# Kernel optimization log

Hardware: AMD Instinct MI355X
Metric: run time of the kernel (lower is better)

## Reference

```python
import jax, jax.numpy as jnp
import numpy as np

BLOCK = 16          # NVFP4 block size along contraction dim
FP4_MAX = 6.0       # max magnitude of E2M1
FP8_MAX = 448.0     # max magnitude of float8_e4m3fn

_LEVELS = jnp.array([0.0, 0.5, 1.0, 1.5, 2.0, 3.0, 4.0, 6.0], dtype=jnp.float32)
_MIDS   = jnp.array([0.25, 0.75, 1.25, 1.75, 2.5, 3.5, 5.0], dtype=jnp.float32)


def quantize_dequant_nvfp4(t, global_scale):
    """Fake-quantize t (last dim % 16 == 0) to NVFP4: per-16-block fp8-e4m3
    scale times global fp32 scale, values snapped to the E2M1 grid."""
    shp = t.shape
    tb = t.reshape(shp[:-1] + (shp[-1] // BLOCK, BLOCK))
    amax = jnp.max(jnp.abs(tb), axis=-1, keepdims=True)
    # per-block scale, quantized to float8_e4m3fn as in TensorCoreNVFP4Layout
    bs = amax / (FP4_MAX * global_scale)
    bs8 = bs.astype(jnp.float8_e4m3fn).astype(jnp.float32)
    scale = bs8 * global_scale                       # effective dequant scale
    v = tb / jnp.maximum(scale, 1e-12)
    sign = jnp.sign(v)
    a = jnp.clip(jnp.abs(v), 0.0, FP4_MAX)
    idx = jnp.sum(a[..., None] > _MIDS, axis=-1)     # nearest E2M1 level
    q = _LEVELS[idx] * sign * scale
    return q.reshape(shp)


def setup_inputs() -> dict:
    key = jax.random.key(0)
    kx, kw, kb = jax.random.split(key, 3)
    x = jax.random.normal(kx, (8192, 4096), dtype=jnp.float32)
    weight = jax.random.normal(kw, (4096, 4096), dtype=jnp.float32) * 0.02
    bias = jax.random.normal(kb, (4096,), dtype=jnp.float32) * 0.02
    # global scales (weight_scale_2 / input_scale): amax / (6 * 448)
    input_scale = jnp.max(jnp.abs(x)) / (FP4_MAX * FP8_MAX)
    weight_scale = jnp.max(jnp.abs(weight)) / (FP4_MAX * FP8_MAX)
    return {"x": x, "weight": weight, "bias": bias,
            "input_scale": input_scale, "weight_scale": weight_scale}


def reference(x, weight, bias, input_scale, weight_scale):
    xq = quantize_dequant_nvfp4(x, input_scale)      # [T, K]
    wq = quantize_dequant_nvfp4(weight, weight_scale)  # [N, K]
    return jnp.einsum('tk,nk->tn', xq, wq) + bias    # F.linear
```

## Files before the change

### kernel.cpp

```cpp
#include <hip/hip_runtime.h>
#include <hip/hip_bf16.h>
#include <stdint.h>

typedef __attribute__((ext_vector_type(8))) __bf16 bf16x8;
typedef __attribute__((ext_vector_type(4))) float f32x4;

#define BM 256
#define BN 256
#define BKT 32
#define RING 4
#define SLOT_BYTES 16384


__device__ __forceinline__ float fp8_e4m3_rne(float x) {
  if (x < 0.015625f) {
    return rintf(x * 512.0f) * 0.001953125f;
  }
  uint32_t u = __float_as_uint(x);
  uint32_t keep = u & 0xFFF00000u;
  uint32_t rem  = u & 0x000FFFFFu;
  uint32_t lsb  = (u >> 20) & 1u;
  if (rem > 0x80000u || (rem == 0x80000u && lsb)) keep += 0x100000u;
  return __uint_as_float(keep);
}

__device__ __forceinline__ float snap_lvl(float a) {
  if (a > 5.0f)  return 6.0f;
  if (a > 3.5f)  return 4.0f;
  if (a > 2.5f)  return 3.0f;
  if (a > 1.75f) return 2.0f;
  if (a > 1.25f) return 1.5f;
  if (a > 0.75f) return 1.0f;
  if (a > 0.25f) return 0.5f;
  return 0.0f;
}

__global__ __launch_bounds__(256) void quant_nvfp4(
    const float* __restrict__ in, unsigned short* __restrict__ out,
    const float* __restrict__ gsp, int nblk) {
  int b = blockIdx.x * 256 + threadIdx.x;
  if (b >= nblk) return;
  float gs = gsp[0];
  const float4* p = reinterpret_cast<const float4*>(in) + (size_t)b * 4;
  float v[16];
#pragma unroll
  for (int i = 0; i < 4; ++i) {
    float4 t4 = p[i];
    v[i * 4 + 0] = t4.x; v[i * 4 + 1] = t4.y;
    v[i * 4 + 2] = t4.z; v[i * 4 + 3] = t4.w;
  }
  float amax = 0.0f;
#pragma unroll
  for (int i = 0; i < 16; ++i) amax = fmaxf(amax, fabsf(v[i]));
  float bs8 = fp8_e4m3_rne(amax / (6.0f * gs));
  float scale = fmaxf(bs8 * gs, 1e-12f);
  unsigned short o[16];
#pragma unroll
  for (int i = 0; i < 16; ++i) {
    float q = v[i] / scale;
    float a = fminf(fabsf(q), 6.0f);
    float val = copysignf(snap_lvl(a) * bs8, q);
    o[i] = (unsigned short)(__float_as_uint(val) >> 16);
  }
  uint4 w0 = make_uint4((uint32_t)o[0] | ((uint32_t)o[1] << 16),
                        (uint32_t)o[2] | ((uint32_t)o[3] << 16),
                        (uint32_t)o[4] | ((uint32_t)o[5] << 16),
                        (uint32_t)o[6] | ((uint32_t)o[7] << 16));
  uint4 w1 = make_uint4((uint32_t)o[8]  | ((uint32_t)o[9]  << 16),
                        (uint32_t)o[10] | ((uint32_t)o[11] << 16),
                        (uint32_t)o[12] | ((uint32_t)o[13] << 16),
                        (uint32_t)o[14] | ((uint32_t)o[15] << 16));
  uint4* op = reinterpret_cast<uint4*>(out + (size_t)b * 16);
  op[0] = w0;
  op[1] = w1;
}


__device__ __forceinline__ void async_lds16(const void* g, void* l) {
  __builtin_amdgcn_global_load_lds((__attribute__((address_space(1))) void*)(g),
                                   (__attribute__((address_space(3))) void*)(l),
                                   16, 0, 0);
}

#define PHASE0(T, DO_STAGE) {                                                  \
    const char* _ab = (const char*)As + ((T) & 3) * SLOT_BYTES;                \
    const char* _bb = (const char*)Bs + ((T) & 3) * SLOT_BYTES;                \
    _Pragma("unroll") for (int mi = 0; mi < 4; ++mi)                           \
      af[mi] = *(const bf16x8*)(_ab + offA[mi]);                               \
    _Pragma("unroll") for (int ni = 0; ni < 4; ++ni)                           \
      bfr[ni] = *(const bf16x8*)(_bb + offB[ni]);                              \
    if (DO_STAGE) {                                                            \
      char* _la = (char*)As + (((T) + 3) & 3) * SLOT_BYTES;                    \
      char* _lb = (char*)Bs + (((T) + 3) & 3) * SLOT_BYTES;                    \
      async_lds16(pA0 + (size_t)((T) + 3) * BKT, _la + lo0);                   \
      async_lds16(pB0 + (size_t)((T) + 3) * BKT, _lb + lo0);                   \
    }                                                                          \
    __builtin_amdgcn_s_barrier();                                              \
    asm volatile("s_waitcnt lgkmcnt(0)" ::: "memory");                         \
    __builtin_amdgcn_sched_barrier(0);                                         \
    __builtin_amdgcn_s_setprio(1);                                             \
    _Pragma("unroll") for (int mi = 0; mi < 4; ++mi)                           \
      _Pragma("unroll") for (int ni = 0; ni < 4; ++ni)                         \
        acc[mi][ni] = __builtin_amdgcn_mfma_f32_16x16x32_bf16(                 \
            af[mi], bfr[ni], acc[mi][ni], 0, 0, 0);                            \
    __builtin_amdgcn_s_setprio(0);                                             \
    __builtin_amdgcn_sched_barrier(0);                                         \
    __builtin_amdgcn_s_barrier();                                              \
  }

#define PHASE1(T, DO_STAGE, VMASM) {                                           \
    const char* _ab = (const char*)As + ((T) & 3) * SLOT_BYTES;                \
    _Pragma("unroll") for (int mi = 0; mi < 4; ++mi)                           \
      af[mi] = *(const bf16x8*)(_ab + offA[4 + mi]);                           \
    if (DO_STAGE) {                                                            \
      char* _la = (char*)As + (((T) + 3) & 3) * SLOT_BYTES;                    \
      char* _lb = (char*)Bs + (((T) + 3) & 3) * SLOT_BYTES;                    \
      async_lds16(pA1 + (size_t)((T) + 3) * BKT, _la + lo1);                   \
      async_lds16(pB1 + (size_t)((T) + 3) * BKT, _lb + lo1);                   \
    }                                                                          \
    VMASM;                                                                     \
    __builtin_amdgcn_s_barrier();                                              \
    asm volatile("s_waitcnt lgkmcnt(0)" ::: "memory");                         \
    __builtin_amdgcn_sched_barrier(0);                                         \
    __builtin_amdgcn_s_setprio(1);                                             \
    _Pragma("unroll") for (int mi = 0; mi < 4; ++mi)                           \
      _Pragma("unroll") for (int ni = 0; ni < 4; ++ni)                         \
        acc[4 + mi][ni] = __builtin_amdgcn_mfma_f32_16x16x32_bf16(             \
            af[mi], bfr[ni], acc[4 + mi][ni], 0, 0, 0);                        \
    __builtin_amdgcn_s_setprio(0);                                             \
    __builtin_amdgcn_sched_barrier(0);                                         \
    __builtin_amdgcn_s_barrier();                                              \
  }

#define STAGE_TILE(s) {                                                        \
    char* _la = (char*)As + ((s) & 3) * SLOT_BYTES;                            \
    char* _lb = (char*)Bs + ((s) & 3) * SLOT_BYTES;                            \
    async_lds16(pA0 + (size_t)(s) * BKT, _la + lo0);                           \
    async_lds16(pB0 + (size_t)(s) * BKT, _lb + lo0);                           \
    async_lds16(pA1 + (size_t)(s) * BKT, _la + lo1);                           \
    async_lds16(pB1 + (size_t)(s) * BKT, _lb + lo1);                           \
  }

__global__ __launch_bounds__(512, 2) void gemm_bt_bf16(
    const unsigned short* __restrict__ A, const unsigned short* __restrict__ B,
    const float* __restrict__ bias, const float* __restrict__ gsx,
    const float* __restrict__ gsw, float* __restrict__ C,
    int M, int N, int K) {
  __shared__ __align__(16) unsigned short As[RING * 8192];
  __shared__ __align__(16) unsigned short Bs[RING * 8192];

  const int t = threadIdx.x;
  const int l = t & 63;
  const int w = t >> 6;
  const int wm = w >> 2, wn = w & 3;

  const int nbn = N / BN;
  const int nwg = (M / BM) * nbn;
  const int cpx = nwg >> 3;
  int bid = blockIdx.x;
  int logical = (bid & 7) * cpx + (bid >> 3);
  const int bm = logical / nbn, bn = logical % nbn;
  const int brow = bm * BM, bcol = bn * BN;

  unsigned int b0 = (unsigned int)t * 16u;
  unsigned int b1 = b0 + 8192u;
  unsigned int bp0 = b0 ^ (((b0 >> 7) & 3u) << 4);
  unsigned int bp1 = b1 ^ (((b1 >> 7) & 3u) << 4);
  const unsigned int lo0 = b0, lo1 = b1;
  const unsigned short* pA0 = A + (size_t)(brow + (bp0 >> 6)) * K + ((bp0 & 63u) >> 1);
  const unsigned short* pA1 = A + (size_t)(brow + (bp1 >> 6)) * K + ((bp1 & 63u) >> 1);
  const unsigned short* pB0 = B + (size_t)(bcol + (bp0 >> 6)) * K + ((bp0 & 63u) >> 1);
  const unsigned short* pB1 = B + (size_t)(bcol + (bp1 >> 6)) * K + ((bp1 & 63u) >> 1);

  unsigned int offA[8], offB[4];
#pragma unroll
  for (int mi = 0; mi < 8; ++mi) {
    unsigned int r = wm * 128 + mi * 16 + (l & 15);
    unsigned int q = r * 64 + ((l >> 4) << 4);
    offA[mi] = q ^ (((q >> 7) & 3u) << 4);
  }
#pragma unroll
  for (int ni = 0; ni < 4; ++ni) {
    unsigned int r = wn * 64 + ni * 16 + (l & 15);
    unsigned int q = r * 64 + ((l >> 4) << 4);
    offB[ni] = q ^ (((q >> 7) & 3u) << 4);
  }

  f32x4 acc[8][4] = {};
  bf16x8 af[4], bfr[4];

  const int nsub = K / BKT;

  STAGE_TILE(0);
  STAGE_TILE(1);
  STAGE_TILE(2);
  asm volatile("s_waitcnt vmcnt(8)" ::: "memory");
  __builtin_amdgcn_s_barrier();

#pragma unroll 1
  for (int T = 0; T < nsub - 3; ++T) {
    PHASE0(T, 1);
    PHASE1(T, 1, asm volatile("s_waitcnt vmcnt(8)" ::: "memory"));
  }
  PHASE0(nsub - 3, 0);
  PHASE1(nsub - 3, 0, asm volatile("s_waitcnt vmcnt(4)" ::: "memory"));
  PHASE0(nsub - 2, 0);
  PHASE1(nsub - 2, 0, asm volatile("s_waitcnt vmcnt(0)" ::: "memory"));
  PHASE0(nsub - 1, 0);
  PHASE1(nsub - 1, 0, (void)0);

  const float gscale = gsx[0] * gsw[0];
  float bias_r[4];
#pragma unroll
  for (int ni = 0; ni < 4; ++ni)
    bias_r[ni] = bias[bcol + wn * 64 + ni * 16 + (l & 15)];
#pragma unroll
  for (int mi = 0; mi < 8; ++mi) {
#pragma unroll
    for (int ni = 0; ni < 4; ++ni) {
#pragma unroll
      for (int r = 0; r < 4; ++r) {
        int row = brow + wm * 128 + mi * 16 + (l >> 4) * 4 + r;
        int col = bcol + wn * 64 + ni * 16 + (l & 15);
        C[(size_t)row * N + col] = acc[mi][ni][r] * gscale + bias_r[ni];
      }
    }
  }
}


extern "C" void kernel_launch(void* const* d_in, const int* in_sizes, int n_in,
                              void* d_out, int out_size, void* d_ws, size_t ws_size,
                              hipStream_t stream) {
  const float* x    = (const float*)d_in[0];
  const float* wgt  = (const float*)d_in[1];
  const float* bias = (const float*)d_in[2];
  const float* isc  = (const float*)d_in[3];
  const float* wsc  = (const float*)d_in[4];
  float* out = (float*)d_out;

  const int N = in_sizes[2];
  const int K = in_sizes[1] / N;
  const int M = in_sizes[0] / K;

  unsigned short* Aq = (unsigned short*)d_ws;
  unsigned short* Bq = Aq + (size_t)M * K;

  int nblkA = M * K / 16;
  quant_nvfp4<<<(nblkA + 255) / 256, 256, 0, stream>>>(x, Aq, isc, nblkA);
  int nblkB = N * K / 16;
  quant_nvfp4<<<(nblkB + 255) / 256, 256, 0, stream>>>(wgt, Bq, wsc, nblkB);

  dim3 grid((M / BM) * (N / BN));
  gemm_bt_bf16<<<grid, 512, 0, stream>>>(Aq, Bq, bias, isc, wsc, out, M, N, K);
}
```

Measured before the change: 305.9 us.

## Interleave LDS fragment reads with MFMAs and drop trailing per-phase barriers

Merges the two per-tile phases into one TILE macro that issues the A and B fragment reads as inline-asm ds_read_b128. It then waits with stepped lgkmcnt(3..0) counts so each group of four MFMAs starts as soon as its A fragment has arrived, instead of waiting for all reads. LDS addresses are precomputed as absolute pointers. The trailing s_barrier after each compute phase is removed, halving barriers per k-step. The risk is a ring-slot reuse hazard, since async loads into the slot read one tile earlier are no longer fenced by a barrier after the consumers' reads finish.

After: 275.1 us. -10.1%, faster.

```diff
diff --git a/kernel.cpp b/kernel.cpp
--- a/kernel.cpp
+++ b/kernel.cpp
@@ -4,6 +4,7 @@
 
 typedef __attribute__((ext_vector_type(8))) __bf16 bf16x8;
 typedef __attribute__((ext_vector_type(4))) float f32x4;
+typedef __attribute__((ext_vector_type(4))) unsigned int u32x4;
 
 #define BM 256
 #define BN 256
@@ -82,55 +83,57 @@
                                    16, 0, 0);
 }
 
-#define PHASE0(T, DO_STAGE) {                                                  \
-    const char* _ab = (const char*)As + ((T) & 3) * SLOT_BYTES;                \
-    const char* _bb = (const char*)Bs + ((T) & 3) * SLOT_BYTES;                \
-    _Pragma("unroll") for (int mi = 0; mi < 4; ++mi)                           \
-      af[mi] = *(const bf16x8*)(_ab + offA[mi]);                               \
-    _Pragma("unroll") for (int ni = 0; ni < 4; ++ni)                           \
-      bfr[ni] = *(const bf16x8*)(_bb + offB[ni]);                              \
+#define DSR(dst, a) asm volatile("ds_read_b128 %0, %1" : "=v"(dst) : "v"(a))
+#define LGKM(N) do { asm volatile("s_waitcnt lgkmcnt(" #N ")" ::: "memory"); \
+                     __builtin_amdgcn_sched_barrier(0); } while (0)
+#define BCB(x) __builtin_bit_cast(bf16x8, x)
+
+#define MF4(mi, ar) do {                                                       \
+    acc[mi][0] = __builtin_amdgcn_mfma_f32_16x16x32_bf16(BCB(ar), BCB(rb0), acc[mi][0], 0, 0, 0); \
+    acc[mi][1] = __builtin_amdgcn_mfma_f32_16x16x32_bf16(BCB(ar), BCB(rb1), acc[mi][1], 0, 0, 0); \
+    acc[mi][2] = __builtin_amdgcn_mfma_f32_16x16x32_bf16(BCB(ar), BCB(rb2), acc[mi][2], 0, 0, 0); \
+    acc[mi][3] = __builtin_amdgcn_mfma_f32_16x16x32_bf16(BCB(ar), BCB(rb3), acc[mi][3], 0, 0, 0); \
+  } while (0)
+
+#define TILE(T, DO_STAGE, VMWAIT) do {                                         \
+    const unsigned soff = (unsigned)(((T) & 3) * SLOT_BYTES);                  \
+    u32x4 rb0, rb1, rb2, rb3, ra0, ra1, ra2, ra3;                              \
+    DSR(rb0, adB[0] + soff); DSR(rb1, adB[1] + soff);                          \
+    DSR(rb2, adB[2] + soff); DSR(rb3, adB[3] + soff);                          \
+    DSR(ra0, adA[0] + soff); DSR(ra1, adA[1] + soff);                          \
+    DSR(ra2, adA[2] + soff); DSR(ra3, adA[3] + soff);                          \
     if (DO_STAGE) {                                                            \
       char* _la = (char*)As + (((T) + 3) & 3) * SLOT_BYTES;                    \
       char* _lb = (char*)Bs + (((T) + 3) & 3) * SLOT_BYTES;                    \
       async_lds16(pA0 + (size_t)((T) + 3) * BKT, _la + lo0);                   \
       async_lds16(pB0 + (size_t)((T) + 3) * BKT, _lb + lo0);                   \
     }                                                                          \
+    __builtin_amdgcn_sched_barrier(0);                                         \
     __builtin_amdgcn_s_barrier();                                              \
-    asm volatile("s_waitcnt lgkmcnt(0)" ::: "memory");                         \
-    __builtin_amdgcn_sched_barrier(0);                                         \
-    __builtin_amdgcn_s_setprio(1);                                             \
-    _Pragma("unroll") for (int mi = 0; mi < 4; ++mi)                           \
-      _Pragma("unroll") for (int ni = 0; ni < 4; ++ni)                         \
-        acc[mi][ni] = __builtin_amdgcn_mfma_f32_16x16x32_bf16(                 \
-            af[mi], bfr[ni], acc[mi][ni], 0, 0, 0);                            \
+    LGKM(3); __builtin_amdgcn_s_setprio(1); MF4(0, ra0);                       \
+    LGKM(2); MF4(1, ra1);                                                      \
+    LGKM(1); MF4(2, ra2);                                                      \
+    LGKM(0); MF4(3, ra3);                                                      \
     __builtin_amdgcn_s_setprio(0);                                             \
     __builtin_amdgcn_sched_barrier(0);                                         \
-    __builtin_amdgcn_s_barrier();                                              \
-  }
-
-#define PHASE1(T, DO_STAGE, VMASM) {                                           \
-    const char* _ab = (const char*)As + ((T) & 3) * SLOT_BYTES;                \
-    _Pragma("unroll") for (int mi = 0; mi < 4; ++mi)                           \
-      af[mi] = *(const bf16x8*)(_ab + offA[4 + mi]);                           \
+    DSR(ra0, adA[4] + soff); DSR(ra1, adA[5] + soff);                          \
+    DSR(ra2, adA[6] + soff); DSR(ra3, adA[7] + soff);                          \
     if (DO_STAGE) {                                                            \
       char* _la = (char*)As + (((T) + 3) & 3) * SLOT_BYTES;                    \
       char* _lb = (char*)Bs + (((T) + 3) & 3) * SLOT_BYTES;                    \
       async_lds16(pA1 + (size_t)((T) + 3) * BKT, _la + lo1);                   \
       async_lds16(pB1 + (size_t)((T) + 3) * BKT, _lb + lo1);                   \
     }                                                                          \
-    VMASM;                                                                     \
+    __builtin_amdgcn_sched_barrier(0);                                         \
+    VMWAIT;                                                                    \
     __builtin_amdgcn_s_barrier();                                              \
-    asm volatile("s_waitcnt lgkmcnt(0)" ::: "memory");                         \
-    __builtin_amdgcn_sched_barrier(0);                                         \
-    __builtin_amdgcn_s_setprio(1);                                             \
-    _Pragma("unroll") for (int mi = 0; mi < 4; ++mi)                           \
-      _Pragma("unroll") for (int ni = 0; ni < 4; ++ni)                         \
-        acc[4 + mi][ni] = __builtin_amdgcn_mfma_f32_16x16x32_bf16(             \
-            af[mi], bfr[ni], acc[4 + mi][ni], 0, 0, 0);                        \
+    LGKM(3); __builtin_amdgcn_s_setprio(1); MF4(4, ra0);                       \
+    LGKM(2); MF4(5, ra1);                                                      \
+    LGKM(1); MF4(6, ra2);                                                      \
+    LGKM(0); MF4(7, ra3);                                                      \
     __builtin_amdgcn_s_setprio(0);                                             \
     __builtin_amdgcn_sched_barrier(0);                                         \
-    __builtin_amdgcn_s_barrier();                                              \
-  }
+  } while (0)
 
 #define STAGE_TILE(s) {                                                        \
     char* _la = (char*)As + ((s) & 3) * SLOT_BYTES;                            \
@@ -172,22 +175,23 @@
   const unsigned short* pB0 = B + (size_t)(bcol + (bp0 >> 6)) * K + ((bp0 & 63u) >> 1);
   const unsigned short* pB1 = B + (size_t)(bcol + (bp1 >> 6)) * K + ((bp1 & 63u) >> 1);
 
-  unsigned int offA[8], offB[4];
+  const unsigned baseAu = (unsigned)(uintptr_t)(&As[0]);
+  const unsigned baseBu = (unsigned)(uintptr_t)(&Bs[0]);
+  unsigned int adA[8], adB[4];
 #pragma unroll
   for (int mi = 0; mi < 8; ++mi) {
     unsigned int r = wm * 128 + mi * 16 + (l & 15);
     unsigned int q = r * 64 + ((l >> 4) << 4);
-    offA[mi] = q ^ (((q >> 7) & 3u) << 4);
+    adA[mi] = baseAu + (q ^ (((q >> 7) & 3u) << 4));
   }
 #pragma unroll
   for (int ni = 0; ni < 4; ++ni) {
     unsigned int r = wn * 64 + ni * 16 + (l & 15);
     unsigned int q = r * 64 + ((l >> 4) << 4);
-    offB[ni] = q ^ (((q >> 7) & 3u) << 4);
+    adB[ni] = baseBu + (q ^ (((q >> 7) & 3u) << 4));
   }
 
   f32x4 acc[8][4] = {};
-  bf16x8 af[4], bfr[4];
 
   const int nsub = K / BKT;
 
@@ -199,15 +203,11 @@
 
 #pragma unroll 1
   for (int T = 0; T < nsub - 3; ++T) {
-    PHASE0(T, 1);
-    PHASE1(T, 1, asm volatile("s_waitcnt vmcnt(8)" ::: "memory"));
-  }
-  PHASE0(nsub - 3, 0);
-  PHASE1(nsub - 3, 0, asm volatile("s_waitcnt vmcnt(4)" ::: "memory"));
-  PHASE0(nsub - 2, 0);
-  PHASE1(nsub - 2, 0, asm volatile("s_waitcnt vmcnt(0)" ::: "memory"));
-  PHASE0(nsub - 1, 0);
-  PHASE1(nsub - 1, 0, (void)0);
+    TILE(T, 1, asm volatile("s_waitcnt vmcnt(8)" ::: "memory"));
+  }
+  TILE(nsub - 3, 0, asm volatile("s_waitcnt vmcnt(4)" ::: "memory"));
+  TILE(nsub - 2, 0, asm volatile("s_waitcnt vmcnt(0)" ::: "memory"));
+  TILE(nsub - 1, 0, (void)0);
 
   const float gscale = gsx[0] * gsw[0];
   float bias_r[4];
```
